# Performance work log

Measured on AMD Instinct MI355X. Metric: run time of the kernel, lower is better.

## Reference

```python
import jax, jax.numpy as jnp
import numpy as np

B, M, DM = 8, 1024, 1024
H, DH, R = 16, 64, 32
DFF, R1, R2, RO = 4096, 512, 512, 512
EPS = 1e-12


def layernorm(x, g, b):
    mu = jnp.mean(x, axis=-1, keepdims=True)
    var = jnp.mean(jnp.square(x - mu), axis=-1, keepdims=True)
    return (x - mu) * jax.lax.rsqrt(var + EPS) * g + b


def setup_inputs() -> dict:
    key = jax.random.key(0)
    ks = jax.random.split(key, 24)
    s = lambda *sh: 1.0 / np.sqrt(sh[-2] if len(sh) > 1 else sh[-1])
    d = {}
    d['x'] = jax.random.normal(ks[0], (B, M, DM), jnp.float32)
    d['mask'] = jnp.zeros((B, M), jnp.float32)  # additive attention mask
    # per-head low-rank QKV factors: P:(H,DM,R), V:(H,R,DH), b:(H,DH)
    for i, nm in enumerate(['q', 'k', 'v']):
        d['P' + nm] = jax.random.normal(ks[1 + 3 * i], (H, DM, R), jnp.float32) * 0.02
        d['V' + nm] = jax.random.normal(ks[2 + 3 * i], (H, R, DH), jnp.float32) * 0.02
        d['b' + nm] = jnp.zeros((H, DH), jnp.float32)
    # attention output projection (low-rank) + LN1
    d['Uo'] = jax.random.normal(ks[10], (DM, RO), jnp.float32) * 0.02
    d['Vo'] = jax.random.normal(ks[11], (RO, DM), jnp.float32) * 0.02
    d['bo_attn'] = jnp.zeros((DM,), jnp.float32)
    d['g1'] = jnp.ones((DM,), jnp.float32)
    d['beta1'] = jnp.zeros((DM,), jnp.float32)
    # FFN low-rank factors + LN2
    d['U1'] = jax.random.normal(ks[12], (DM, R1), jnp.float32) * 0.02
    d['V1'] = jax.random.normal(ks[13], (R1, DFF), jnp.float32) * 0.02
    d['b1'] = jnp.zeros((DFF,), jnp.float32)
    d['U2'] = jax.random.normal(ks[14], (DFF, R2), jnp.float32) * 0.02
    d['V2'] = jax.random.normal(ks[15], (R2, DM), jnp.float32) * 0.02
    d['b2'] = jnp.zeros((DM,), jnp.float32)
    d['g2'] = jnp.ones((DM,), jnp.float32)
    d['beta2'] = jnp.zeros((DM,), jnp.float32)
    return d


def reference(x, mask, Pq, Vq, bq, Pk, Vk, bk, Pv, Vv, bv,
              Uo, Vo, bo_attn, g1, beta1,
              U1, V1, b1, U2, V2, b2, g2, beta2):
    # low-rank Q/K/V: x @ P -> (B,H,M,R), then @ V -> (B,H,M,DH), + bias
    def qkv(P, V, b):
        tmp = jnp.einsum('bmd,hdr->bhmr', x, P)
        return jnp.einsum('bhmr,hre->bhme', tmp, V) + b[None, :, None, :]

    Q = qkv(Pq, Vq, bq)
    K = qkv(Pk, Vk, bk)
    V = qkv(Pv, Vv, bv)
    scale = 1.0 / jnp.sqrt(jnp.asarray(DH, x.dtype))
    scores = jnp.einsum('bhme,bhne->bhmn', Q, K) * scale
    scores = scores + mask[:, None, None, :]  # additive mask broadcast over heads/queries
    probs = jax.nn.softmax(scores, axis=-1)
    attn = jnp.einsum('bhmn,bhne->bhme', probs, V)  # (B,H,M,DH)
    attn = attn.transpose(0, 2, 1, 3).reshape(attn.shape[0], attn.shape[2], -1)  # (B,M,DM)
    x1 = layernorm(x + (attn @ Uo) @ Vo + bo_attn, g1, beta1)
    # FFN: GELU((x1 @ U1) @ V1 + b1) @ U2 @ V2 + b2 (flashsvd_ffn semantics)
    mid = x1 @ U1
    hidden = jax.nn.gelu(mid @ V1 + b1, approximate=False)
    y = (hidden @ U2) @ V2 + b2
    return layernorm(x1 + y, g2, beta2)
```

## Files before the change

kernel.cpp:

```cpp
#include <hip/hip_runtime.h>
#include <hip/hip_bf16.h>
#include <math.h>

typedef unsigned short u16;
typedef unsigned int u32;
typedef __attribute__((ext_vector_type(8))) short bf16x8;
typedef __attribute__((ext_vector_type(4))) float f32x4;

#define B_ 8
#define M_ 1024
#define DM_ 1024
#define H_ 16
#define DH_ 64
#define NR_ 8192

__device__ __forceinline__ u16 f2bf(float f) {
    unsigned u = __float_as_uint(f);
    u += 0x7FFFu + ((u >> 16) & 1u);
    return (u16)(u >> 16);
}

__device__ __forceinline__ void gload16(const void* g, void* l) {
    __builtin_amdgcn_global_load_lds(
        (const __attribute__((address_space(1))) void*)g,
        (__attribute__((address_space(3))) void*)l, 16, 0, 0);
}

__global__ __launch_bounds__(256) void conv_bf16(const float* __restrict__ in,
                                                 u16* __restrict__ out) {
    int i = (blockIdx.x * 256 + threadIdx.x) * 4;
    float4 v = *reinterpret_cast<const float4*>(in + i);
    unsigned long long p = (unsigned long long)f2bf(v.x)
                         | ((unsigned long long)f2bf(v.y) << 16)
                         | ((unsigned long long)f2bf(v.z) << 32)
                         | ((unsigned long long)f2bf(v.w) << 48);
    *reinterpret_cast<unsigned long long*>(out + i) = p;
}

__global__ __launch_bounds__(256) void prep_p(const float* __restrict__ P,
                                              u16* __restrict__ Pt) {
    __shared__ float Ps[128][33];
    const int h = blockIdx.x, kc = blockIdx.y * 128, tid = threadIdx.x;
#pragma unroll
    for (int i = 0; i < 16; ++i) {
        int e = tid + i * 256;
        int kk = e >> 5, r = e & 31;
        Ps[kk][r] = P[(size_t)h * 32768 + (size_t)(kc + kk) * 32 + r];
    }
    __syncthreads();
#pragma unroll
    for (int i = 0; i < 16; ++i) {
        int e = tid + i * 256;
        int r = e >> 7, k = e & 127;
        Pt[(size_t)(h * 32 + r) * 1024 + kc + k] = f2bf(Ps[k][r]);
    }
}

__global__ __launch_bounds__(256) void prep_f(const float* __restrict__ V,
                                              u16* __restrict__ Ft) {
    __shared__ float Vs[32][65];
    const int h = blockIdx.x, tid = threadIdx.x;
#pragma unroll
    for (int i = 0; i < 8; ++i) {
        int e = tid + i * 256;
        int r = e >> 6, c = e & 63;
        Vs[r][c] = V[(size_t)h * 2048 + r * 64 + c];
    }
    __syncthreads();
#pragma unroll
    for (int i = 0; i < 8; ++i) {
        int idx = tid + i * 256;
        int e = idx >> 5, r = idx & 31;
        Ft[(size_t)h * 2560 + e * 40 + r] = f2bf(Vs[r][e]);
    }
}

__global__ __launch_bounds__(256) void transpose_w(const float* __restrict__ in,
                                                   u16* __restrict__ out,
                                                   int R, int C) {
    __shared__ float t[64][65];
    const int rb = blockIdx.y * 64, cb = blockIdx.x * 64, tid = threadIdx.x;
#pragma unroll
    for (int i = 0; i < 16; ++i) {
        int e = tid + i * 256;
        int r = e >> 6, c = e & 63;
        t[r][c] = in[(size_t)(rb + r) * C + cb + c];
    }
    __syncthreads();
#pragma unroll
    for (int i = 0; i < 16; ++i) {
        int e = tid + i * 256;
        int r = e >> 6, c = e & 63;
        out[(size_t)(cb + r) * R + rb + c] = f2bf(t[c][r]);
    }
}

template <int EPI, int NF>
__global__ __launch_bounds__(256) void gemm_bf16(const u16* __restrict__ A,
                                                 const u16* __restrict__ Bt,
                                                 const float* __restrict__ bias,
                                                 void* __restrict__ Cout,
                                                 int K, int N) {
    constexpr int BN = NF * 32;
    __shared__ u16 As[128 * 64];
    __shared__ u16 Bs[BN * 64];
    const int tid = threadIdx.x;
    const int lane = tid & 63, wv = tid >> 6;

    const int NX = gridDim.x;
    const int flat = blockIdx.x + blockIdx.y * NX;
    const int q = (NX * gridDim.y) >> 3;
    const int nid = (flat & 7) * q + (flat >> 3);
    const int row0 = (nid / NX) * 128, col0 = (nid % NX) * BN;

    const int frow = lane & 15, fk8 = lane >> 4;
    const int wm = (wv >> 1) * 64, wn = (wv & 1) * (BN / 2);

    f32x4 acc[4][NF];
    const f32x4 z4 = {0.f, 0.f, 0.f, 0.f};
#pragma unroll
    for (int i = 0; i < 4; ++i)
#pragma unroll
        for (int j = 0; j < NF; ++j) acc[i][j] = z4;

    for (int k0 = 0; k0 < K; k0 += 64) {
#pragma unroll
        for (int i = 0; i < 4; ++i) {
            int rr = (i * 4 + wv) * 8 + (lane >> 3);
            int cc = ((lane & 7) ^ (rr & 7)) * 8;
            gload16(A + (size_t)(row0 + rr) * K + k0 + cc,
                    (char*)As + (i * 4 + wv) * 1024);
        }
#pragma unroll
        for (int i = 0; i < NF; ++i) {
            int rr = (i * 4 + wv) * 8 + (lane >> 3);
            int cc = ((lane & 7) ^ (rr & 7)) * 8;
            gload16(Bt + (size_t)(col0 + rr) * K + k0 + cc,
                    (char*)Bs + (i * 4 + wv) * 1024);
        }
        asm volatile("s_waitcnt vmcnt(0)" ::: "memory");
        __syncthreads();
#pragma unroll
        for (int kf = 0; kf < 2; ++kf) {
            bf16x8 af[4], bfr[NF];
#pragma unroll
            for (int mf = 0; mf < 4; ++mf) {
                int r = wm + mf * 16 + frow;
                int c16 = (kf * 4 + fk8) ^ (r & 7);
                af[mf] = *reinterpret_cast<const bf16x8*>((char*)As + r * 128 + c16 * 16);
            }
#pragma unroll
            for (int nf = 0; nf < NF; ++nf) {
                int r = wn + nf * 16 + frow;
                int c16 = (kf * 4 + fk8) ^ (r & 7);
                bfr[nf] = *reinterpret_cast<const bf16x8*>((char*)Bs + r * 128 + c16 * 16);
            }
#pragma unroll
            for (int mf = 0; mf < 4; ++mf)
#pragma unroll
                for (int nf = 0; nf < NF; ++nf)
                    acc[mf][nf] = __builtin_amdgcn_mfma_f32_16x16x32_bf16(
                        af[mf], bfr[nf], acc[mf][nf], 0, 0, 0);
        }
        __syncthreads();
    }

    const int orow = fk8 * 4, ocol = frow;
#pragma unroll
    for (int mf = 0; mf < 4; ++mf)
#pragma unroll
        for (int nf = 0; nf < NF; ++nf)
#pragma unroll
            for (int j = 0; j < 4; ++j) {
                int row = row0 + wm + mf * 16 + orow + j;
                int col = col0 + wn + nf * 16 + ocol;
                float v = acc[mf][nf][j];
                if (EPI == 2) {
                    v += bias[col];
                    v = 0.5f * v * (1.f + erff(v * 0.70710678118f));
                    ((u16*)Cout)[(size_t)row * N + col] = f2bf(v);
                } else if (EPI == 3) {
                    ((float*)Cout)[(size_t)row * N + col] = v;
                } else {
                    ((u16*)Cout)[(size_t)row * N + col] = f2bf(v);
                }
            }
}

__global__ __launch_bounds__(256) void gemm_db(const u16* __restrict__ A,
                                               const u16* __restrict__ Bt,
                                               u16* __restrict__ Cout,
                                               int K, int N) {
    __shared__ u16 As[2][128 * 64];
    __shared__ u16 Bs[2][64 * 64];
    const int tid = threadIdx.x;
    const int lane = tid & 63, wv = tid >> 6;

    const int NX = gridDim.x;
    const int flat = blockIdx.x + blockIdx.y * NX;
    const int q = (NX * gridDim.y) >> 3;
    const int nid = (flat & 7) * q + (flat >> 3);
    const int row0 = (nid / NX) * 128, col0 = (nid % NX) * 64;

    const int frow = lane & 15, fk8 = lane >> 4;
    const int wm = (wv >> 1) * 64, wn = (wv & 1) * 32;

    f32x4 acc[4][2];
    const f32x4 z4 = {0.f, 0.f, 0.f, 0.f};
#pragma unroll
    for (int i = 0; i < 4; ++i) {
        acc[i][0] = z4;
        acc[i][1] = z4;
    }

    const int srr = (lane >> 3);
    const int scc = (lane & 7);

#pragma unroll
    for (int i = 0; i < 4; ++i) {
        int rr = (i * 4 + wv) * 8 + srr;
        int cc = (scc ^ (rr & 7)) * 8;
        gload16(A + (size_t)(row0 + rr) * K + cc, (char*)&As[0][0] + (i * 4 + wv) * 1024);
    }
#pragma unroll
    for (int i = 0; i < 2; ++i) {
        int rr = (i * 4 + wv) * 8 + srr;
        int cc = (scc ^ (rr & 7)) * 8;
        gload16(Bt + (size_t)(col0 + rr) * K + cc, (char*)&Bs[0][0] + (i * 4 + wv) * 1024);
    }

    int cur = 0;
    for (int k0 = 0; k0 < K; k0 += 64) {
        __syncthreads();
        if (k0 + 64 < K) {
            int kn = k0 + 64;
#pragma unroll
            for (int i = 0; i < 4; ++i) {
                int rr = (i * 4 + wv) * 8 + srr;
                int cc = (scc ^ (rr & 7)) * 8;
                gload16(A + (size_t)(row0 + rr) * K + kn + cc,
                        (char*)&As[cur ^ 1][0] + (i * 4 + wv) * 1024);
            }
#pragma unroll
            for (int i = 0; i < 2; ++i) {
                int rr = (i * 4 + wv) * 8 + srr;
                int cc = (scc ^ (rr & 7)) * 8;
                gload16(Bt + (size_t)(col0 + rr) * K + kn + cc,
                        (char*)&Bs[cur ^ 1][0] + (i * 4 + wv) * 1024);
            }
        }
#pragma unroll
        for (int kf = 0; kf < 2; ++kf) {
            bf16x8 af[4], bfr[2];
#pragma unroll
            for (int mf = 0; mf < 4; ++mf) {
                int r = wm + mf * 16 + frow;
                int c16 = (kf * 4 + fk8) ^ (r & 7);
                af[mf] = *reinterpret_cast<const bf16x8*>((char*)&As[cur][0] + r * 128 + c16 * 16);
            }
#pragma unroll
            for (int nf = 0; nf < 2; ++nf) {
                int r = wn + nf * 16 + frow;
                int c16 = (kf * 4 + fk8) ^ (r & 7);
                bfr[nf] = *reinterpret_cast<const bf16x8*>((char*)&Bs[cur][0] + r * 128 + c16 * 16);
            }
#pragma unroll
            for (int mf = 0; mf < 4; ++mf)
#pragma unroll
                for (int nf = 0; nf < 2; ++nf)
                    acc[mf][nf] = __builtin_amdgcn_mfma_f32_16x16x32_bf16(
                        af[mf], bfr[nf], acc[mf][nf], 0, 0, 0);
        }
        cur ^= 1;
    }

#pragma unroll
    for (int mf = 0; mf < 4; ++mf)
#pragma unroll
        for (int nf = 0; nf < 2; ++nf)
#pragma unroll
            for (int j = 0; j < 4; ++j) {
                int row = row0 + wm + mf * 16 + fk8 * 4 + j;
                int col = col0 + wn + nf * 16 + frow;
                Cout[(size_t)row * N + col] = f2bf(acc[mf][nf][j]);
            }
}

__global__ __launch_bounds__(256) void qkv_s2(const u16* __restrict__ Tmp,
                                              const u16* __restrict__ Ftq,
                                              const u16* __restrict__ Ftk,
                                              const u16* __restrict__ Ftv,
                                              const float* __restrict__ bq,
                                              const float* __restrict__ bk,
                                              const float* __restrict__ bv,
                                              u16* __restrict__ Q,
                                              u16* __restrict__ K,
                                              u16* __restrict__ V) {
    __shared__ u16 Ts[64 * 104];
    const int m0 = blockIdx.x * 64, h = blockIdx.y, tid = threadIdx.x;
    const int lane = tid & 63, wv = tid >> 6;
    const int frow = lane & 15, fk8 = lane >> 4;

    {
        const int row = tid >> 2, seg = tid & 3;
#pragma unroll
        for (int sect = 0; sect < 3; ++sect) {
            int off = sect * 512 + h * 32;
            uint4 v = *reinterpret_cast<const uint4*>(
                Tmp + (size_t)(m0 + row) * 1536 + off + seg * 8);
            *reinterpret_cast<uint4*>(&Ts[row * 104 + sect * 32 + seg * 8]) = v;
        }
    }
    __syncthreads();

    const u16* Fts[3] = {Ftq, Ftk, Ftv};
    const float* bs[3] = {bq, bk, bv};
    u16* outs[3] = {Q, K, V};

    f32x4 acc[3][4];
    const f32x4 z4 = {0.f, 0.f, 0.f, 0.f};
#pragma unroll
    for (int f = 0; f < 3; ++f) {
        bf16x8 a = *reinterpret_cast<const bf16x8*>(
            &Ts[(wv * 16 + frow) * 104 + f * 32 + fk8 * 8]);
#pragma unroll
        for (int nf = 0; nf < 4; ++nf) {
            int e = nf * 16 + frow;
            bf16x8 b = *reinterpret_cast<const bf16x8*>(
                Fts[f] + (size_t)h * 2560 + e * 40 + fk8 * 8);
            acc[f][nf] = __builtin_amdgcn_mfma_f32_16x16x32_bf16(a, b, z4, 0, 0, 0);
        }
    }

    const int bb = m0 >> 10;
#pragma unroll
    for (int f = 0; f < 3; ++f)
#pragma unroll
        for (int nf = 0; nf < 4; ++nf) {
            int e = nf * 16 + frow;
            float bias = bs[f][h * 64 + e];
#pragma unroll
            for (int j = 0; j < 4; ++j) {
                int m = m0 + wv * 16 + fk8 * 4 + j;
                outs[f][(((size_t)(bb * 16 + h) << 10) + (m & 1023)) * 64 + e] =
                    f2bf(acc[f][nf][j] + bias);
            }
        }
}

__global__ __launch_bounds__(256) void attn_mfma(const u16* __restrict__ Q,
                                                 const u16* __restrict__ K,
                                                 const u16* __restrict__ V,
                                                 const float* __restrict__ mask,
                                                 u16* __restrict__ O) {
    __shared__ u16 Qs[64 * 64];
    __shared__ u16 Ks[64 * 64];
    __shared__ u16 Vt[64 * 64];
    __shared__ u16 Pw[4 * 16 * 72];
    const int flat = blockIdx.x;
    const int nid = (flat & 7) * 256 + (flat >> 3);
    const int hb = nid >> 4, qt = nid & 15;
    const int b = hb >> 4, h = hb & 15;
    const int tid = threadIdx.x, lane = tid & 63, wv = tid >> 6;
    const int frow = lane & 15, fk8 = lane >> 4;
    const size_t base = (size_t)hb * 65536;
    const float LOG2E = 1.44269504089f;

#pragma unroll
    for (int i = 0; i < 2; ++i) {
        int rr = (i * 4 + wv) * 8 + (lane >> 3);
        int cc = ((lane & 7) ^ (rr & 7)) * 8;
        gload16(Q + base + (size_t)(qt * 64 + rr) * 64 + cc,
                (char*)Qs + (i * 4 + wv) * 1024);
    }
    asm volatile("s_waitcnt vmcnt(0)" ::: "memory");
    __syncthreads();

    bf16x8 qfrag[2];
#pragma unroll
    for (int kf = 0; kf < 2; ++kf) {
        int qr = wv * 16 + frow;
        int qc16 = (kf * 4 + fk8) ^ (qr & 7);
        qfrag[kf] = *reinterpret_cast<const bf16x8*>((char*)Qs + qr * 128 + qc16 * 16);
    }

    float m_i = -1e30f, l_i = 0.f;
    const f32x4 z4 = {0.f, 0.f, 0.f, 0.f};
    f32x4 o_acc[4];
#pragma unroll
    for (int nf = 0; nf < 4; ++nf) o_acc[nf] = z4;

    const int vkey = (tid & 31) * 2, vd0 = (tid >> 5) * 8;
    u32* pw32 = reinterpret_cast<u32*>(Pw);

    for (int kt = 0; kt < 16; ++kt) {
        __syncthreads();
#pragma unroll
        for (int i = 0; i < 2; ++i) {
            int rr = (i * 4 + wv) * 8 + (lane >> 3);
            int cc = ((lane & 7) ^ (rr & 7)) * 8;
            gload16(K + base + (size_t)(kt * 64 + rr) * 64 + cc,
                    (char*)Ks + (i * 4 + wv) * 1024);
        }
        {
            const u16* vsrc = V + base + (size_t)(kt * 64 + vkey) * 64 + vd0;
            uint4 va = *reinterpret_cast<const uint4*>(vsrc);
            uint4 vb = *reinterpret_cast<const uint4*>(vsrc + 64);
            u16 k0[8], k1[8];
            *reinterpret_cast<uint4*>(k0) = va;
            *reinterpret_cast<uint4*>(k1) = vb;
#pragma unroll
            for (int i = 0; i < 8; ++i) {
                int d = vd0 + i;
                int slot = (vkey >> 3) ^ (d & 7);
                u32 w = (u32)k0[i] | ((u32)k1[i] << 16);
                reinterpret_cast<u32*>(Vt)[(d * 64 + slot * 8 + (vkey & 7)) >> 1] = w;
            }
        }
        asm volatile("s_waitcnt vmcnt(0)" ::: "memory");
        __syncthreads();

        f32x4 sacc[4];
#pragma unroll
        for (int nf = 0; nf < 4; ++nf) sacc[nf] = z4;
        __builtin_amdgcn_s_setprio(1);
#pragma unroll
        for (int kf = 0; kf < 2; ++kf) {
#pragma unroll
            for (int nf = 0; nf < 4; ++nf) {
                int kr = nf * 16 + frow;
                int kc16 = (kf * 4 + fk8) ^ (kr & 7);
                bf16x8 ak = *reinterpret_cast<const bf16x8*>((char*)Ks + kr * 128 + kc16 * 16);
                sacc[nf] = __builtin_amdgcn_mfma_f32_16x16x32_bf16(ak, qfrag[kf], sacc[nf], 0, 0, 0);
            }
        }
        __builtin_amdgcn_s_setprio(0);

        float tval[4][4];
        float tmax = -1e30f;
#pragma unroll
        for (int nf = 0; nf < 4; ++nf) {
            float4 mk = *reinterpret_cast<const float4*>(
                mask + b * M_ + kt * 64 + nf * 16 + fk8 * 4);
            float t0 = fmaf(sacc[nf][0], 0.125f, mk.x);
            float t1 = fmaf(sacc[nf][1], 0.125f, mk.y);
            float t2 = fmaf(sacc[nf][2], 0.125f, mk.z);
            float t3 = fmaf(sacc[nf][3], 0.125f, mk.w);
            tval[nf][0] = t0; tval[nf][1] = t1; tval[nf][2] = t2; tval[nf][3] = t3;
            tmax = fmaxf(tmax, fmaxf(fmaxf(t0, t1), fmaxf(t2, t3)));
        }
        tmax = fmaxf(tmax, __shfl_xor(tmax, 16));
        tmax = fmaxf(tmax, __shfl_xor(tmax, 32));

        if (__any(tmax > m_i + 8.f)) {
            float mnew = fmaxf(m_i, tmax);
            float c = exp2f((m_i - mnew) * LOG2E);
            m_i = mnew;
            l_i *= c;
#pragma unroll
            for (int j = 0; j < 4; ++j) {
                float cj = __shfl(c, fk8 * 4 + j);
#pragma unroll
                for (int nf = 0; nf < 4; ++nf) o_acc[nf][j] *= cj;
            }
        }

        const float ml = m_i * LOG2E;
        float rs = 0.f;
#pragma unroll
        for (int nf = 0; nf < 4; ++nf) {
            float p0 = exp2f(fmaf(tval[nf][0], LOG2E, -ml));
            float p1 = exp2f(fmaf(tval[nf][1], LOG2E, -ml));
            float p2 = exp2f(fmaf(tval[nf][2], LOG2E, -ml));
            float p3 = exp2f(fmaf(tval[nf][3], LOG2E, -ml));
            rs += (p0 + p1) + (p2 + p3);
            u32 w0 = (__float_as_uint(p0) >> 16) | (__float_as_uint(p1) & 0xFFFF0000u);
            u32 w1 = (__float_as_uint(p2) >> 16) | (__float_as_uint(p3) & 0xFFFF0000u);
            int pidx = wv * 576 + frow * 36 + nf * 8 + fk8 * 2;
            pw32[pidx] = w0;
            pw32[pidx + 1] = w1;
        }
        rs += __shfl_xor(rs, 16);
        rs += __shfl_xor(rs, 32);
        l_i += rs;

        __builtin_amdgcn_s_setprio(1);
#pragma unroll
        for (int kf = 0; kf < 2; ++kf) {
            bf16x8 ap = *reinterpret_cast<const bf16x8*>(
                (char*)Pw + wv * 2304 + frow * 144 + kf * 64 + fk8 * 16);
#pragma unroll
            for (int nf = 0; nf < 4; ++nf) {
                int vr = nf * 16 + frow;
                int vc16 = (kf * 4 + fk8) ^ (vr & 7);
                bf16x8 bv = *reinterpret_cast<const bf16x8*>((char*)Vt + vr * 128 + vc16 * 16);
                o_acc[nf] = __builtin_amdgcn_mfma_f32_16x16x32_bf16(ap, bv, o_acc[nf], 0, 0, 0);
            }
        }
        __builtin_amdgcn_s_setprio(0);
    }

#pragma unroll
    for (int j = 0; j < 4; ++j) {
        float lq = __shfl(l_i, fk8 * 4 + j);
        float inv = 1.f / lq;
        int grow = qt * 64 + wv * 16 + fk8 * 4 + j;
        size_t obase = ((size_t)(b * M_ + grow)) * DM_ + h * 64;
#pragma unroll
        for (int nf = 0; nf < 4; ++nf)
            O[obase + nf * 16 + frow] = f2bf(o_acc[nf][j] * inv);
    }
}

template <bool WBF>
__global__ __launch_bounds__(256) void ln_kernel(const float* __restrict__ y,
                                                 const float* __restrict__ res,
                                                 const float* __restrict__ bias,
                                                 const float* __restrict__ g,
                                                 const float* __restrict__ beta,
                                                 float* __restrict__ outf,
                                                 u16* __restrict__ outb) {
    __shared__ float red[2][4];
    const int row = blockIdx.x, tid = threadIdx.x;
    const size_t base = (size_t)row * 1024 + tid * 4;
    float4 v = *reinterpret_cast<const float4*>(y + base);
    float4 r = *reinterpret_cast<const float4*>(res + base);
    float4 bb = *reinterpret_cast<const float4*>(bias + tid * 4);
    v.x += r.x + bb.x; v.y += r.y + bb.y; v.z += r.z + bb.z; v.w += r.w + bb.w;
    float sum = v.x + v.y + v.z + v.w;
    float sq = v.x * v.x + v.y * v.y + v.z * v.z + v.w * v.w;
#pragma unroll
    for (int off = 32; off; off >>= 1) {
        sum += __shfl_down(sum, off);
        sq += __shfl_down(sq, off);
    }
    if ((tid & 63) == 0) { red[0][tid >> 6] = sum; red[1][tid >> 6] = sq; }
    __syncthreads();
    sum = red[0][0] + red[0][1] + red[0][2] + red[0][3];
    sq = red[1][0] + red[1][1] + red[1][2] + red[1][3];
    float mu = sum * (1.f / 1024.f);
    float var = sq * (1.f / 1024.f) - mu * mu;
    float rstd = rsqrtf(var + 1e-12f);
    float4 gg = *reinterpret_cast<const float4*>(g + tid * 4);
    float4 be = *reinterpret_cast<const float4*>(beta + tid * 4);
    float4 o;
    o.x = (v.x - mu) * rstd * gg.x + be.x;
    o.y = (v.y - mu) * rstd * gg.y + be.y;
    o.z = (v.z - mu) * rstd * gg.z + be.z;
    o.w = (v.w - mu) * rstd * gg.w + be.w;
    *reinterpret_cast<float4*>(outf + base) = o;
    if (WBF) {
        unsigned long long p = (unsigned long long)f2bf(o.x)
                             | ((unsigned long long)f2bf(o.y) << 16)
                             | ((unsigned long long)f2bf(o.z) << 32)
                             | ((unsigned long long)f2bf(o.w) << 48);
        *reinterpret_cast<unsigned long long*>(outb + base) = p;
    }
}

extern "C" void kernel_launch(void* const* d_in, const int* in_sizes, int n_in,
                              void* d_out, int out_size, void* d_ws, size_t ws_size,
                              hipStream_t stream) {
    const float* x    = (const float*)d_in[0];
    const float* mask = (const float*)d_in[1];
    const float* Pq   = (const float*)d_in[2];
    const float* Vq   = (const float*)d_in[3];
    const float* bq   = (const float*)d_in[4];
    const float* Pk   = (const float*)d_in[5];
    const float* Vk   = (const float*)d_in[6];
    const float* bk   = (const float*)d_in[7];
    const float* Pv   = (const float*)d_in[8];
    const float* Vv   = (const float*)d_in[9];
    const float* bv   = (const float*)d_in[10];
    const float* Uo   = (const float*)d_in[11];
    const float* Vo   = (const float*)d_in[12];
    const float* bo   = (const float*)d_in[13];
    const float* g1   = (const float*)d_in[14];
    const float* be1  = (const float*)d_in[15];
    const float* U1   = (const float*)d_in[16];
    const float* V1   = (const float*)d_in[17];
    const float* b1   = (const float*)d_in[18];
    const float* U2   = (const float*)d_in[19];
    const float* V2   = (const float*)d_in[20];
    const float* b2   = (const float*)d_in[21];
    const float* g2   = (const float*)d_in[22];
    const float* be2  = (const float*)d_in[23];
    float* out = (float*)d_out;

    const size_t MB = 1048576;
    char* ws = (char*)d_ws;
    u16* Pt  = (u16*)(ws + 0);
    u16* Ftq = (u16*)(ws + 3 * MB);
    u16* Ftk = (u16*)(ws + 3 * MB + 131072);
    u16* Ftv = (u16*)(ws + 3 * MB + 262144);
    u16* Uot = (u16*)(ws + 4 * MB);
    u16* Vot = (u16*)(ws + 5 * MB);
    u16* U1t = (u16*)(ws + 6 * MB);
    u16* V1t = (u16*)(ws + 7 * MB);
    u16* U2t = (u16*)(ws + 11 * MB);
    u16* V2t = (u16*)(ws + 15 * MB);
    u16* Xb  = (u16*)(ws + 16 * MB);
    u16* Tmp = (u16*)(ws + 32 * MB);
    u16* Qb  = (u16*)(ws + 56 * MB);
    u16* Kb  = (u16*)(ws + 72 * MB);
    u16* Vb  = (u16*)(ws + 88 * MB);
    u16* Ob  = (u16*)(ws + 104 * MB);
    u16* Hb  = (u16*)(ws + 32 * MB);
    float* Yf = (float*)(ws + 56 * MB);
    u16* Tb  = (u16*)(ws + 96 * MB);
    float* X1f = (float*)(ws + 120 * MB);

    conv_bf16<<<8192, 256, 0, stream>>>(x, Xb);
    prep_p<<<dim3(16, 8), 256, 0, stream>>>(Pq, Pt);
    prep_p<<<dim3(16, 8), 256, 0, stream>>>(Pk, Pt + 512 * 1024);
    prep_p<<<dim3(16, 8), 256, 0, stream>>>(Pv, Pt + 1024 * 1024);
    prep_f<<<16, 256, 0, stream>>>(Vq, Ftq);
    prep_f<<<16, 256, 0, stream>>>(Vk, Ftk);
    prep_f<<<16, 256, 0, stream>>>(Vv, Ftv);
    transpose_w<<<dim3(8, 16), 256, 0, stream>>>(Uo, Uot, 1024, 512);
    transpose_w<<<dim3(16, 8), 256, 0, stream>>>(Vo, Vot, 512, 1024);
    transpose_w<<<dim3(8, 16), 256, 0, stream>>>(U1, U1t, 1024, 512);
    transpose_w<<<dim3(64, 8), 256, 0, stream>>>(V1, V1t, 512, 4096);
    transpose_w<<<dim3(8, 64), 256, 0, stream>>>(U2, U2t, 4096, 512);
    transpose_w<<<dim3(16, 8), 256, 0, stream>>>(V2, V2t, 512, 1024);

    gemm_bf16<0, 4><<<dim3(12, 64), 256, 0, stream>>>(Xb, Pt, nullptr, Tmp, 1024, 1536);
    qkv_s2<<<dim3(128, 16), 256, 0, stream>>>(Tmp, Ftq, Ftk, Ftv, bq, bk, bv, Qb, Kb, Vb);

    attn_mfma<<<2048, 256, 0, stream>>>(Qb, Kb, Vb, mask, Ob);

    gemm_db<<<dim3(8, 64), 256, 0, stream>>>(Ob, Uot, Tb, 1024, 512);
    gemm_bf16<3, 4><<<dim3(8, 64), 256, 0, stream>>>(Tb, Vot, nullptr, Yf, 512, 1024);
    ln_kernel<true><<<8192, 256, 0, stream>>>(Yf, x, bo, g1, be1, X1f, Xb);

    gemm_db<<<dim3(8, 64), 256, 0, stream>>>(Xb, U1t, Tb, 1024, 512);
    gemm_bf16<2, 4><<<dim3(32, 64), 256, 0, stream>>>(Tb, V1t, b1, Hb, 512, 4096);
    gemm_db<<<dim3(8, 64), 256, 0, stream>>>(Hb, U2t, Tb, 4096, 512);
    gemm_bf16<3, 4><<<dim3(8, 64), 256, 0, stream>>>(Tb, V2t, nullptr, Yf, 512, 1024);
    ln_kernel<false><<<8192, 256, 0, stream>>>(Yf, X1f, b2, g2, be2, out, nullptr);
}
```

Before: 378.8 us.

## Fuse weight prep launches and use transpose LDS reads for attention V

Merges the input conversion and all weight transpose/prep kernels into one launch with block-range dispatch, so thirteen small launches become one. In attention, V tiles are now loaded straight into LDS with async global_load_lds in a blocked layout, and read back with ds_read_b64_tr_b16 transpose reads. This replaces the register-based manual transpose and its scattered LDS writes. The P buffer is shrunk and XOR-swizzled, Q staging reuses the K buffer to cut LDS use, and the probabilities are packed with perm. The inline asm adds explicit waitcnt and sched barriers, which may limit overlap.

```diff
diff --git a/kernel.cpp b/kernel.cpp
--- a/kernel.cpp
+++ b/kernel.cpp
@@ -6,6 +6,8 @@
 typedef unsigned int u32;
 typedef __attribute__((ext_vector_type(8))) short bf16x8;
 typedef __attribute__((ext_vector_type(4))) float f32x4;
+typedef __attribute__((ext_vector_type(2))) unsigned int u32x2;
+typedef __attribute__((ext_vector_type(4))) unsigned int u32x4;
 
 #define B_ 8
 #define M_ 1024
@@ -26,21 +28,27 @@
         (__attribute__((address_space(3))) void*)l, 16, 0, 0);
 }
 
-__global__ __launch_bounds__(256) void conv_bf16(const float* __restrict__ in,
-                                                 u16* __restrict__ out) {
-    int i = (blockIdx.x * 256 + threadIdx.x) * 4;
-    float4 v = *reinterpret_cast<const float4*>(in + i);
-    unsigned long long p = (unsigned long long)f2bf(v.x)
-                         | ((unsigned long long)f2bf(v.y) << 16)
-                         | ((unsigned long long)f2bf(v.z) << 32)
-                         | ((unsigned long long)f2bf(v.w) << 48);
-    *reinterpret_cast<unsigned long long*>(out + i) = p;
-}
-
-__global__ __launch_bounds__(256) void prep_p(const float* __restrict__ P,
-                                              u16* __restrict__ Pt) {
-    __shared__ float Ps[128][33];
-    const int h = blockIdx.x, kc = blockIdx.y * 128, tid = threadIdx.x;
+__device__ __forceinline__ u32 lds_addr(const void* p) {
+    return (u32)(uintptr_t)(const __attribute__((address_space(3))) void*)p;
+}
+
+__device__ void conv_dev(const float* __restrict__ in, u16* __restrict__ out,
+                         int bid, int tid) {
+#pragma unroll
+    for (int j = 0; j < 4; ++j) {
+        int i = bid * 4096 + j * 1024 + tid * 4;
+        float4 v = *reinterpret_cast<const float4*>(in + i);
+        unsigned long long p = (unsigned long long)f2bf(v.x)
+                             | ((unsigned long long)f2bf(v.y) << 16)
+                             | ((unsigned long long)f2bf(v.z) << 32)
+                             | ((unsigned long long)f2bf(v.w) << 48);
+        *reinterpret_cast<unsigned long long*>(out + i) = p;
+    }
+}
+
+__device__ void prep_p_dev(const float* __restrict__ P, u16* __restrict__ Pt,
+                           int h, int kc, int tid, float* sm) {
+    float (*Ps)[33] = (float(*)[33])sm;
 #pragma unroll
     for (int i = 0; i < 16; ++i) {
         int e = tid + i * 256;
@@ -56,10 +64,9 @@
     }
 }
 
-__global__ __launch_bounds__(256) void prep_f(const float* __restrict__ V,
-                                              u16* __restrict__ Ft) {
-    __shared__ float Vs[32][65];
-    const int h = blockIdx.x, tid = threadIdx.x;
+__device__ void prep_f_dev(const float* __restrict__ V, u16* __restrict__ Ft,
+                           int h, int tid, float* sm) {
+    float (*Vs)[65] = (float(*)[65])sm;
 #pragma unroll
     for (int i = 0; i < 8; ++i) {
         int e = tid + i * 256;
@@ -75,11 +82,10 @@
     }
 }
 
-__global__ __launch_bounds__(256) void transpose_w(const float* __restrict__ in,
-                                                   u16* __restrict__ out,
-                                                   int R, int C) {
-    __shared__ float t[64][65];
-    const int rb = blockIdx.y * 64, cb = blockIdx.x * 64, tid = threadIdx.x;
+__device__ void transp_dev(const float* __restrict__ in, u16* __restrict__ out,
+                           int R, int C, int bx, int by, int tid, float* sm) {
+    float (*t)[65] = (float(*)[65])sm;
+    const int rb = by * 64, cb = bx * 64;
 #pragma unroll
     for (int i = 0; i < 16; ++i) {
         int e = tid + i * 256;
@@ -92,6 +98,52 @@
         int e = tid + i * 256;
         int r = e >> 6, c = e & 63;
         out[(size_t)(cb + r) * R + rb + c] = f2bf(t[c][r]);
+    }
+}
+
+__global__ __launch_bounds__(256) void prep_all(
+    const float* __restrict__ x,
+    const float* __restrict__ Pq, const float* __restrict__ Pk, const float* __restrict__ Pv,
+    const float* __restrict__ Vq, const float* __restrict__ Vk, const float* __restrict__ Vv,
+    const float* __restrict__ Uo, const float* __restrict__ Vo,
+    const float* __restrict__ U1, const float* __restrict__ V1,
+    const float* __restrict__ U2, const float* __restrict__ V2,
+    u16* __restrict__ Xb, u16* __restrict__ Pt,
+    u16* __restrict__ Ftq, u16* __restrict__ Ftk, u16* __restrict__ Ftv,
+    u16* __restrict__ Uot, u16* __restrict__ Vot,
+    u16* __restrict__ U1t, u16* __restrict__ V1t,
+    u16* __restrict__ U2t, u16* __restrict__ V2t) {
+    __shared__ float smem[4224];
+    const int bid = blockIdx.x, tid = threadIdx.x;
+    if (bid < 2048) {
+        conv_dev(x, Xb, bid, tid);
+    } else if (bid < 2432) {
+        int t = bid - 2048, which = t >> 7, tt = t & 127;
+        const float* P = which == 0 ? Pq : (which == 1 ? Pk : Pv);
+        prep_p_dev(P, Pt + (size_t)which * 524288, tt >> 3, (tt & 7) * 128, tid, smem);
+    } else if (bid < 2480) {
+        int t = bid - 2432, which = t >> 4;
+        const float* V = which == 0 ? Vq : (which == 1 ? Vk : Vv);
+        u16* F = which == 0 ? Ftq : (which == 1 ? Ftk : Ftv);
+        prep_f_dev(V, F, t & 15, tid, smem);
+    } else if (bid < 2608) {
+        int t = bid - 2480;
+        transp_dev(Uo, Uot, 1024, 512, t & 7, t >> 3, tid, smem);
+    } else if (bid < 2736) {
+        int t = bid - 2608;
+        transp_dev(Vo, Vot, 512, 1024, t & 15, t >> 4, tid, smem);
+    } else if (bid < 2864) {
+        int t = bid - 2736;
+        transp_dev(U1, U1t, 1024, 512, t & 7, t >> 3, tid, smem);
+    } else if (bid < 3376) {
+        int t = bid - 2864;
+        transp_dev(V1, V1t, 512, 4096, t & 63, t >> 6, tid, smem);
+    } else if (bid < 3888) {
+        int t = bid - 3376;
+        transp_dev(U2, U2t, 4096, 512, t & 7, t >> 3, tid, smem);
+    } else {
+        int t = bid - 3888;
+        transp_dev(V2, V2t, 512, 1024, t & 15, t >> 4, tid, smem);
     }
 }
 
@@ -353,10 +405,9 @@
                                                  const u16* __restrict__ V,
                                                  const float* __restrict__ mask,
                                                  u16* __restrict__ O) {
-    __shared__ u16 Qs[64 * 64];
-    __shared__ u16 Ks[64 * 64];
-    __shared__ u16 Vt[64 * 64];
-    __shared__ u16 Pw[4 * 16 * 72];
+    __shared__ u16 Ks[4096];
+    __shared__ u16 Vt[4096];
+    __shared__ u16 Pw[4096];
     const int flat = blockIdx.x;
     const int nid = (flat & 7) * 256 + (flat >> 3);
     const int hb = nid >> 4, qt = nid & 15;
@@ -365,83 +416,81 @@
     const int frow = lane & 15, fk8 = lane >> 4;
     const size_t base = (size_t)hb * 65536;
     const float LOG2E = 1.44269504089f;
+    const int srr = lane >> 3, scc = lane & 7;
 
 #pragma unroll
     for (int i = 0; i < 2; ++i) {
-        int rr = (i * 4 + wv) * 8 + (lane >> 3);
-        int cc = ((lane & 7) ^ (rr & 7)) * 8;
+        int rr = (i * 4 + wv) * 8 + srr;
+        int cc = (scc ^ (rr & 7)) * 8;
         gload16(Q + base + (size_t)(qt * 64 + rr) * 64 + cc,
-                (char*)Qs + (i * 4 + wv) * 1024);
+                (char*)Ks + (i * 4 + wv) * 1024);
     }
     asm volatile("s_waitcnt vmcnt(0)" ::: "memory");
     __syncthreads();
-
     bf16x8 qfrag[2];
 #pragma unroll
     for (int kf = 0; kf < 2; ++kf) {
         int qr = wv * 16 + frow;
-        int qc16 = (kf * 4 + fk8) ^ (qr & 7);
-        qfrag[kf] = *reinterpret_cast<const bf16x8*>((char*)Qs + qr * 128 + qc16 * 16);
-    }
+        int c16 = (kf * 4 + fk8) ^ (qr & 7);
+        qfrag[kf] = *reinterpret_cast<const bf16x8*>((char*)Ks + qr * 128 + c16 * 16);
+    }
+
+    int voff[2];
+#pragma unroll
+    for (int i = 0; i < 2; ++i) {
+        int c = (i * 4 + wv) * 64 + lane;
+        int kb = c >> 5, db = (c >> 3) & 3, kr = (c >> 1) & 3, hf = c & 1;
+        voff[i] = (kb * 4 + kr) * 64 + db * 16 + hf * 8;
+    }
+
+    u32 vta[4];
+    {
+        u32 vt0 = lds_addr(Vt) + fk8 * 1024 + frow * 2;
+#pragma unroll
+        for (int nf = 0; nf < 4; ++nf) vta[nf] = vt0 + nf * 128;
+    }
+
+    char* pwW = (char*)Pw + wv * 2048 + frow * 128 + (fk8 & 1) * 8;
+    char* pwR = (char*)Pw + wv * 2048 + frow * 128;
+    const float* mrow = mask + b * M_;
 
     float m_i = -1e30f, l_i = 0.f;
     const f32x4 z4 = {0.f, 0.f, 0.f, 0.f};
-    f32x4 o_acc[4];
-#pragma unroll
-    for (int nf = 0; nf < 4; ++nf) o_acc[nf] = z4;
-
-    const int vkey = (tid & 31) * 2, vd0 = (tid >> 5) * 8;
-    u32* pw32 = reinterpret_cast<u32*>(Pw);
+    f32x4 o_acc[4] = {z4, z4, z4, z4};
 
     for (int kt = 0; kt < 16; ++kt) {
         __syncthreads();
 #pragma unroll
         for (int i = 0; i < 2; ++i) {
-            int rr = (i * 4 + wv) * 8 + (lane >> 3);
-            int cc = ((lane & 7) ^ (rr & 7)) * 8;
+            int rr = (i * 4 + wv) * 8 + srr;
+            int cc = (scc ^ (rr & 7)) * 8;
             gload16(K + base + (size_t)(kt * 64 + rr) * 64 + cc,
                     (char*)Ks + (i * 4 + wv) * 1024);
         }
-        {
-            const u16* vsrc = V + base + (size_t)(kt * 64 + vkey) * 64 + vd0;
-            uint4 va = *reinterpret_cast<const uint4*>(vsrc);
-            uint4 vb = *reinterpret_cast<const uint4*>(vsrc + 64);
-            u16 k0[8], k1[8];
-            *reinterpret_cast<uint4*>(k0) = va;
-            *reinterpret_cast<uint4*>(k1) = vb;
-#pragma unroll
-            for (int i = 0; i < 8; ++i) {
-                int d = vd0 + i;
-                int slot = (vkey >> 3) ^ (d & 7);
-                u32 w = (u32)k0[i] | ((u32)k1[i] << 16);
-                reinterpret_cast<u32*>(Vt)[(d * 64 + slot * 8 + (vkey & 7)) >> 1] = w;
-            }
-        }
+#pragma unroll
+        for (int i = 0; i < 2; ++i)
+            gload16(V + base + kt * 4096 + voff[i], (char*)Vt + (i * 4 + wv) * 1024);
         asm volatile("s_waitcnt vmcnt(0)" ::: "memory");
         __syncthreads();
 
-        f32x4 sacc[4];
-#pragma unroll
-        for (int nf = 0; nf < 4; ++nf) sacc[nf] = z4;
+        f32x4 sacc[4] = {z4, z4, z4, z4};
         __builtin_amdgcn_s_setprio(1);
 #pragma unroll
-        for (int kf = 0; kf < 2; ++kf) {
+        for (int kf = 0; kf < 2; ++kf)
 #pragma unroll
             for (int nf = 0; nf < 4; ++nf) {
                 int kr = nf * 16 + frow;
-                int kc16 = (kf * 4 + fk8) ^ (kr & 7);
-                bf16x8 ak = *reinterpret_cast<const bf16x8*>((char*)Ks + kr * 128 + kc16 * 16);
+                int c16 = (kf * 4 + fk8) ^ (kr & 7);
+                bf16x8 ak = *reinterpret_cast<const bf16x8*>((char*)Ks + kr * 128 + c16 * 16);
                 sacc[nf] = __builtin_amdgcn_mfma_f32_16x16x32_bf16(ak, qfrag[kf], sacc[nf], 0, 0, 0);
             }
-        }
         __builtin_amdgcn_s_setprio(0);
 
         float tval[4][4];
         float tmax = -1e30f;
 #pragma unroll
         for (int nf = 0; nf < 4; ++nf) {
-            float4 mk = *reinterpret_cast<const float4*>(
-                mask + b * M_ + kt * 64 + nf * 16 + fk8 * 4);
+            float4 mk = *reinterpret_cast<const float4*>(mrow + kt * 64 + nf * 16 + fk8 * 4);
             float t0 = fmaf(sacc[nf][0], 0.125f, mk.x);
             float t1 = fmaf(sacc[nf][1], 0.125f, mk.y);
             float t2 = fmaf(sacc[nf][2], 0.125f, mk.z);
@@ -474,30 +523,63 @@
             float p2 = exp2f(fmaf(tval[nf][2], LOG2E, -ml));
             float p3 = exp2f(fmaf(tval[nf][3], LOG2E, -ml));
             rs += (p0 + p1) + (p2 + p3);
-            u32 w0 = (__float_as_uint(p0) >> 16) | (__float_as_uint(p1) & 0xFFFF0000u);
-            u32 w1 = (__float_as_uint(p2) >> 16) | (__float_as_uint(p3) & 0xFFFF0000u);
-            int pidx = wv * 576 + frow * 36 + nf * 8 + fk8 * 2;
-            pw32[pidx] = w0;
-            pw32[pidx + 1] = w1;
+            u32 w0 = __builtin_amdgcn_perm(__float_as_uint(p1), __float_as_uint(p0), 0x07060302u);
+            u32 w1 = __builtin_amdgcn_perm(__float_as_uint(p3), __float_as_uint(p2), 0x07060302u);
+            u32x2 wp = {w0, w1};
+            *reinterpret_cast<u32x2*>(pwW + (((nf * 2 + (fk8 >> 1)) ^ (frow & 7)) * 16)) = wp;
         }
         rs += __shfl_xor(rs, 16);
         rs += __shfl_xor(rs, 32);
         l_i += rs;
 
-        __builtin_amdgcn_s_setprio(1);
 #pragma unroll
         for (int kf = 0; kf < 2; ++kf) {
-            bf16x8 ap = *reinterpret_cast<const bf16x8*>(
-                (char*)Pw + wv * 2304 + frow * 144 + kf * 64 + fk8 * 16);
-#pragma unroll
-            for (int nf = 0; nf < 4; ++nf) {
-                int vr = nf * 16 + frow;
-                int vc16 = (kf * 4 + fk8) ^ (vr & 7);
-                bf16x8 bv = *reinterpret_cast<const bf16x8*>((char*)Vt + vr * 128 + vc16 * 16);
-                o_acc[nf] = __builtin_amdgcn_mfma_f32_16x16x32_bf16(ap, bv, o_acc[nf], 0, 0, 0);
-            }
-        }
-        __builtin_amdgcn_s_setprio(0);
+            bf16x8 ap = *reinterpret_cast<const bf16x8*>(pwR + (((kf * 4 + fk8) ^ (frow & 7)) * 16));
+            u32x2 r0, r1, r2, r3, r4, r5, r6, r7;
+            if (kf == 0) {
+                asm volatile("ds_read_b64_tr_b16 %0, %1" : "=&v"(r0) : "v"(vta[0]));
+                asm volatile("ds_read_b64_tr_b16 %0, %1 offset:512" : "=&v"(r1) : "v"(vta[0]));
+                asm volatile("ds_read_b64_tr_b16 %0, %1" : "=&v"(r2) : "v"(vta[1]));
+                asm volatile("ds_read_b64_tr_b16 %0, %1 offset:512" : "=&v"(r3) : "v"(vta[1]));
+                asm volatile("ds_read_b64_tr_b16 %0, %1" : "=&v"(r4) : "v"(vta[2]));
+                asm volatile("ds_read_b64_tr_b16 %0, %1 offset:512" : "=&v"(r5) : "v"(vta[2]));
+                asm volatile("ds_read_b64_tr_b16 %0, %1" : "=&v"(r6) : "v"(vta[3]));
+                asm volatile("ds_read_b64_tr_b16 %0, %1 offset:512" : "=&v"(r7) : "v"(vta[3]));
+            } else {
+                asm volatile("ds_read_b64_tr_b16 %0, %1 offset:4096" : "=&v"(r0) : "v"(vta[0]));
+                asm volatile("ds_read_b64_tr_b16 %0, %1 offset:4608" : "=&v"(r1) : "v"(vta[0]));
+                asm volatile("ds_read_b64_tr_b16 %0, %1 offset:4096" : "=&v"(r2) : "v"(vta[1]));
+                asm volatile("ds_read_b64_tr_b16 %0, %1 offset:4608" : "=&v"(r3) : "v"(vta[1]));
+                asm volatile("ds_read_b64_tr_b16 %0, %1 offset:4096" : "=&v"(r4) : "v"(vta[2]));
+                asm volatile("ds_read_b64_tr_b16 %0, %1 offset:4608" : "=&v"(r5) : "v"(vta[2]));
+                asm volatile("ds_read_b64_tr_b16 %0, %1 offset:4096" : "=&v"(r6) : "v"(vta[3]));
+                asm volatile("ds_read_b64_tr_b16 %0, %1 offset:4608" : "=&v"(r7) : "v"(vta[3]));
+            }
+            asm volatile("s_waitcnt lgkmcnt(0)" ::: "memory");
+            __builtin_amdgcn_sched_barrier(0);
+            __builtin_amdgcn_s_setprio(1);
+            {
+                u32x4 vv = {r0.x, r0.y, r1.x, r1.y};
+                bf16x8 f; __builtin_memcpy(&f, &vv, 16);
+                o_acc[0] = __builtin_amdgcn_mfma_f32_16x16x32_bf16(ap, f, o_acc[0], 0, 0, 0);
+            }
+            {
+                u32x4 vv = {r2.x, r2.y, r3.x, r3.y};
+                bf16x8 f; __builtin_memcpy(&f, &vv, 16);
+                o_acc[1] = __builtin_amdgcn_mfma_f32_16x16x32_bf16(ap, f, o_acc[1], 0, 0, 0);
+            }
+            {
+                u32x4 vv = {r4.x, r4.y, r5.x, r5.y};
+                bf16x8 f; __builtin_memcpy(&f, &vv, 16);
+                o_acc[2] = __builtin_amdgcn_mfma_f32_16x16x32_bf16(ap, f, o_acc[2], 0, 0, 0);
+            }
+            {
+                u32x4 vv = {r6.x, r6.y, r7.x, r7.y};
+                bf16x8 f; __builtin_memcpy(&f, &vv, 16);
+                o_acc[3] = __builtin_amdgcn_mfma_f32_16x16x32_bf16(ap, f, o_acc[3], 0, 0, 0);
+            }
+            __builtin_amdgcn_s_setprio(0);
+        }
     }
 
 #pragma unroll
@@ -610,19 +692,10 @@
     u16* Tb  = (u16*)(ws + 96 * MB);
     float* X1f = (float*)(ws + 120 * MB);
 
-    conv_bf16<<<8192, 256, 0, stream>>>(x, Xb);
-    prep_p<<<dim3(16, 8), 256, 0, stream>>>(Pq, Pt);
-    prep_p<<<dim3(16, 8), 256, 0, stream>>>(Pk, Pt + 512 * 1024);
-    prep_p<<<dim3(16, 8), 256, 0, stream>>>(Pv, Pt + 1024 * 1024);
-    prep_f<<<16, 256, 0, stream>>>(Vq, Ftq);
-    prep_f<<<16, 256, 0, stream>>>(Vk, Ftk);
-    prep_f<<<16, 256, 0, stream>>>(Vv, Ftv);
-    transpose_w<<<dim3(8, 16), 256, 0, stream>>>(Uo, Uot, 1024, 512);
-    transpose_w<<<dim3(16, 8), 256, 0, stream>>>(Vo, Vot, 512, 1024);
-    transpose_w<<<dim3(8, 16), 256, 0, stream>>>(U1, U1t, 1024, 512);
-    transpose_w<<<dim3(64, 8), 256, 0, stream>>>(V1, V1t, 512, 4096);
-    transpose_w<<<dim3(8, 64), 256, 0, stream>>>(U2, U2t, 4096, 512);
-    transpose_w<<<dim3(16, 8), 256, 0, stream>>>(V2, V2t, 512, 1024);
+    prep_all<<<4016, 256, 0, stream>>>(x, Pq, Pk, Pv, Vq, Vk, Vv,
+                                       Uo, Vo, U1, V1, U2, V2,
+                                       Xb, Pt, Ftq, Ftk, Ftv,
+                                       Uot, Vot, U1t, V1t, U2t, V2t);
 
     gemm_bf16<0, 4><<<dim3(12, 64), 256, 0, stream>>>(Xb, Pt, nullptr, Tmp, 1024, 1536);
     qkv_s2<<<dim3(128, 16), 256, 0, stream>>>(Tmp, Ftq, Ftk, Ftv, bq, bk, bv, Qb, Kb, Vb);
```

Result: faster. 347.5 us (-8.3%).
